# Performance work log

Hardware: AMD Instinct MI355X
Metric: run time of the kernel (lower is better)

The kernel has to match this reference:

```python
import jax, jax.numpy as jnp
import numpy as np

D_MODEL = 2048
NHEADS = 16
NOPE = 128
ROPE = 64
VDIM = 128
QLORA = 1536
KVLORA = 512
QHD = NOPE + ROPE  # 192
B, T = 1, 4096


def rms_norm(x, w):
    # torch.nn.RMSNorm with eps=None uses finfo(dtype).eps
    eps = jnp.finfo(x.dtype).eps
    var = jnp.mean(x * x, axis=-1, keepdims=True)
    return x * jax.lax.rsqrt(var + eps) * w


def rope_cos_sin(T, dim):
    freqs = 1.0 / (10000.0 ** (jnp.arange(0, dim, 2, dtype=jnp.float32) / dim))
    ang = jnp.arange(T, dtype=jnp.float32)[:, None] * freqs[None, :]  # (T, dim/2)
    return jnp.cos(ang), jnp.sin(ang)


def apply_rope(x, cos, sin):
    # interleaved RoPE: even/odd channel pairs rotated
    xe = x[..., 0::2]
    xo = x[..., 1::2]
    re = xe * cos - xo * sin
    ro = xo * cos + xe * sin
    return jnp.stack([re, ro], axis=-1).reshape(x.shape)


def setup_inputs() -> dict:
    key = jax.random.key(0)
    ks = jax.random.split(key, 6)
    s = 0.02
    return {
        "x": jax.random.normal(ks[0], (B, T, D_MODEL), jnp.float32),
        "Wqa": jax.random.normal(ks[1], (D_MODEL, QLORA), jnp.float32) * s,
        "q_ln_w": jnp.ones((QLORA,), jnp.float32),
        "Wqb": jax.random.normal(ks[2], (QLORA, NHEADS * QHD), jnp.float32) * s,
        "Wkva": jax.random.normal(ks[3], (D_MODEL, KVLORA + ROPE), jnp.float32) * s,
        "kv_ln_w": jnp.ones((KVLORA,), jnp.float32),
        "Wkvb": jax.random.normal(ks[4], (KVLORA, NHEADS * (NOPE + VDIM)), jnp.float32) * s,
        "Wo": jax.random.normal(ks[5], (NHEADS * VDIM, D_MODEL), jnp.float32) * s,
    }


def reference(x, Wqa, q_ln_w, Wqb, Wkva, kv_ln_w, Wkvb, Wo):
    Bx, Tx, _ = x.shape
    cos, sin = rope_cos_sin(Tx, ROPE)  # (T, ROPE/2)

    # Low-rank Q path
    q = rms_norm(x @ Wqa, q_ln_w) @ Wqb
    q = q.reshape(Bx, Tx, NHEADS, QHD).transpose(0, 2, 1, 3)  # (B,H,T,QHD)
    q_nope = q[..., :NOPE]
    q_rope = apply_rope(q[..., NOPE:], cos, sin)  # (B,H,T,ROPE)

    # Compressed KV path + shared rope key
    kv = x @ Wkva
    kv_c = kv[..., :KVLORA]  # (B,T,KVLORA) latent cache
    k_rope = apply_rope(kv[..., KVLORA:], cos, sin)  # (B,T,ROPE), head-shared

    kvb = (rms_norm(kv_c, kv_ln_w) @ Wkvb).reshape(Bx, Tx, NHEADS, NOPE + VDIM)
    k_nope = kvb[..., :NOPE].transpose(0, 2, 1, 3)  # (B,H,T,NOPE)
    v = kvb[..., NOPE:].transpose(0, 2, 1, 3)       # (B,H,T,VDIM)

    # Scores split into nope part + head-shared rope part (avoids expanding k_rope to H heads)
    scale = 1.0 / jnp.sqrt(jnp.float32(QHD))
    s = jnp.einsum('bhqd,bhkd->bhqk', q_nope, k_nope)
    s = s + jnp.einsum('bhqd,bkd->bhqk', q_rope, k_rope)
    s = s * scale

    mask = jnp.tril(jnp.ones((Tx, Tx), dtype=bool))
    s = jnp.where(mask, s, -jnp.inf)
    a = jax.nn.softmax(s, axis=-1)

    o = jnp.einsum('bhqk,bhkd->bhqd', a, v)
    o = o.transpose(0, 2, 1, 3).reshape(Bx, Tx, NHEADS * VDIM)
    return o @ Wo
```

## Files before the change

kernel.cpp:

```cpp
#include <hip/hip_runtime.h>
#include <hip/hip_bf16.h>

typedef __attribute__((ext_vector_type(8))) short short8;
typedef __attribute__((ext_vector_type(4))) float f32x4;

#define GLDS16(gp, lp)                                                         \
  __builtin_amdgcn_global_load_lds(                                            \
      (const __attribute__((address_space(1))) void*)(gp),                     \
      (__attribute__((address_space(3))) void*)(lp), 16, 0, 0)

static __device__ __forceinline__ unsigned int pack_bf16(float a, float b) {
  __hip_bfloat16 ba = __float2bfloat16(a), bb = __float2bfloat16(b);
  unsigned short ua = *reinterpret_cast<unsigned short*>(&ba);
  unsigned short ub = *reinterpret_cast<unsigned short*>(&bb);
  return (unsigned int)ua | ((unsigned int)ub << 16);
}

static __device__ __forceinline__ int xcd_swz(int linear, int nwg) {
  return (linear & 7) * (nwg >> 3) + (linear >> 3);
}

__global__ __launch_bounds__(256) void cast_bf16_kernel(
    const float* __restrict__ in, __hip_bfloat16* __restrict__ out, int n4)
{
  int i = blockIdx.x * 256 + threadIdx.x;
  if (i < n4) {
    float4 v = ((const float4*)in)[i];
    out[(size_t)i * 4 + 0] = __float2bfloat16(v.x);
    out[(size_t)i * 4 + 1] = __float2bfloat16(v.y);
    out[(size_t)i * 4 + 2] = __float2bfloat16(v.z);
    out[(size_t)i * 4 + 3] = __float2bfloat16(v.w);
  }
}

__global__ void transpose_cast_kernel(const float* __restrict__ in,
                                      __hip_bfloat16* __restrict__ out,
                                      int K, int N, int Npad)
{
  __shared__ float tile[32][33];
  int n0 = blockIdx.x * 32, k0 = blockIdx.y * 32;
  int tx = threadIdx.x, ty = threadIdx.y;
  #pragma unroll
  for (int i = ty; i < 32; i += 8) {
    int k = k0 + i, n = n0 + tx;
    tile[i][tx] = (n < N) ? in[(size_t)k * N + n] : 0.f;
  }
  __syncthreads();
  #pragma unroll
  for (int i = ty; i < 32; i += 8) {
    int n = n0 + i, k = k0 + tx;
    if (n < Npad) out[(size_t)n * K + k] = __float2bfloat16(tile[tx][i]);
  }
}

__global__ void rope_tab_kernel(float* __restrict__ cs, float* __restrict__ sn)
{
  int t = blockIdx.x, i = threadIdx.x;
  float freq = powf(10000.f, -2.f * (float)i / 64.f);
  float ang = (float)t * freq;
  cs[t * 32 + i] = cosf(ang);
  sn[t * 32 + i] = sinf(ang);
}

#define GEMM_MAIN(A, BT, Kdim)                                                 \
  __shared__ __hip_bfloat16 As[128 * 32];                                      \
  __shared__ __hip_bfloat16 Bs[128 * 32];                                      \
  const int tid = threadIdx.x;                                                 \
  const int wave = tid >> 6, lane = tid & 63;                                  \
  const int wr = wave >> 1, wc = wave & 1;                                     \
  const int lq = lane & 15, grp = lane >> 4;                                   \
  const int nwg = gridDim.x * gridDim.y;                                       \
  const int orig = xcd_swz(blockIdx.y * gridDim.x + blockIdx.x, nwg);          \
  const int row0 = (orig / gridDim.x) * 128;                                   \
  const int col0 = (orig % gridDim.x) * 128;                                   \
  const f32x4 z4 = {0.f, 0.f, 0.f, 0.f};                                       \
  f32x4 acc[4][4];                                                             \
  _Pragma("unroll") for (int i = 0; i < 4; i++)                                \
      _Pragma("unroll") for (int j = 0; j < 4; j++) acc[i][j] = z4;            \
  for (int k0 = 0; k0 < (Kdim); k0 += 32) {                                    \
    _Pragma("unroll") for (int i = 0; i < 2; i++) {                            \
      const int t = wave + 4 * i;                                              \
      const int c = t * 64 + lane;                                             \
      const int cr = c >> 2;                                                   \
      const int ko = (c & 3) << 3;                                             \
      GLDS16((A) + (size_t)(row0 + cr) * (Kdim) + (k0 + ko), (char*)As + t * 1024); \
      GLDS16((BT) + (size_t)(col0 + cr) * (Kdim) + (k0 + ko), (char*)Bs + t * 1024);\
    }                                                                          \
    __syncthreads();                                                           \
    short8 af[4], bfr[4];                                                      \
    _Pragma("unroll") for (int mm = 0; mm < 4; mm++)                           \
      af[mm] = *(const short8*)((const short*)As + ((wr * 64 + mm * 16 + lq) * 32 + grp * 8)); \
    _Pragma("unroll") for (int nn = 0; nn < 4; nn++)                           \
      bfr[nn] = *(const short8*)((const short*)Bs + ((wc * 64 + nn * 16 + lq) * 32 + grp * 8));\
    _Pragma("unroll") for (int mm = 0; mm < 4; mm++)                           \
      _Pragma("unroll") for (int nn = 0; nn < 4; nn++)                         \
        acc[mm][nn] = __builtin_amdgcn_mfma_f32_16x16x32_bf16(af[mm], bfr[nn], acc[mm][nn], 0, 0, 0); \
    __syncthreads();                                                           \
  }

__global__ __launch_bounds__(256) void gemm_bt_kernel(
    const __hip_bfloat16* __restrict__ A,
    const __hip_bfloat16* __restrict__ BT,
    float* __restrict__ C, int M, int N, int K)
{
  GEMM_MAIN(A, BT, K)
  #pragma unroll
  for (int mm = 0; mm < 4; mm++)
    #pragma unroll
    for (int nn = 0; nn < 4; nn++) {
      const int row = row0 + wr * 64 + mm * 16 + grp * 4;
      const int col = col0 + wc * 64 + nn * 16 + lq;
      float* Cp = C + (size_t)row * N + col;
      #pragma unroll
      for (int rr = 0; rr < 4; rr++) Cp[(size_t)rr * N] = acc[mm][nn][rr];
    }
}

#define GEMM256_MAIN(Aptr, BTptr, Kdim)                                        \
  __shared__ __align__(16) char Ab[2][32768];                                  \
  __shared__ __align__(16) char Bb[2][32768];                                  \
  const int tid = threadIdx.x;                                                 \
  const int wid = tid >> 6, lane = tid & 63;                                   \
  const int wm = wid >> 2, wn = wid & 3;                                       \
  const int lq = lane & 15, grp = lane >> 4;                                   \
  const int nwg = gridDim.x * gridDim.y;                                       \
  const int orig = xcd_swz(blockIdx.y * gridDim.x + blockIdx.x, nwg);          \
  const int row0 = (orig / gridDim.x) * 256;                                   \
  const int col0 = (orig % gridDim.x) * 256;                                   \
  const size_t K2 = (size_t)(Kdim) * 2;                                        \
  const char* pa[4]; const char* pb[4]; int ldst[4];                           \
  _Pragma("unroll") for (int i = 0; i < 4; i++) {                              \
    int L = i * 8192 + tid * 16;                                               \
    int r = L >> 7;                                                            \
    int csw = (L & 127) ^ ((r & 7) << 4);                                      \
    ldst[i] = L;                                                               \
    pa[i] = (const char*)(Aptr) + (size_t)(row0 + r) * K2 + csw;               \
    pb[i] = (const char*)(BTptr) + (size_t)(col0 + r) * K2 + csw;              \
  }                                                                            \
  const int xm = (lq & 7) << 4;                                                \
  const f32x4 z4 = {0.f, 0.f, 0.f, 0.f};                                       \
  f32x4 acc[8][4];                                                             \
  _Pragma("unroll") for (int i = 0; i < 8; i++)                                \
    _Pragma("unroll") for (int j = 0; j < 4; j++) acc[i][j] = z4;              \
  const int nt = (Kdim) >> 6;                                                  \
  _Pragma("unroll") for (int i = 0; i < 4; i++) {                              \
    GLDS16(pa[i], &Ab[0][0] + ldst[i]);                                        \
    GLDS16(pb[i], &Bb[0][0] + ldst[i]);                                        \
  }                                                                            \
  for (int t = 0; t < nt; ++t) {                                               \
    const int b = t & 1;                                                       \
    if (t + 1 < nt) {                                                          \
      const size_t koff = (size_t)(t + 1) * 128;                               \
      _Pragma("unroll") for (int i = 0; i < 4; i++) {                          \
        GLDS16(pa[i] + koff, &Ab[b ^ 1][0] + ldst[i]);                         \
        GLDS16(pb[i] + koff, &Bb[b ^ 1][0] + ldst[i]);                         \
      }                                                                        \
      asm volatile("s_waitcnt vmcnt(8)" ::: "memory");                         \
    } else {                                                                   \
      asm volatile("s_waitcnt vmcnt(0)" ::: "memory");                         \
    }                                                                          \
    __builtin_amdgcn_sched_barrier(0);                                         \
    __builtin_amdgcn_s_barrier();             \
    __builtin_amdgcn_sched_barrier(0);                                         \
    const char* Ar = &Ab[b][0];                                                \
    const char* Br = &Bb[b][0];                                                \
    short8 bfr[4][2];                                                          \
    _Pragma("unroll") for (int n = 0; n < 4; n++)                              \
      _Pragma("unroll") for (int ks = 0; ks < 2; ks++)                         \
        bfr[n][ks] = *(const short8*)(Br + (wn * 64 + n * 16 + lq) * 128 +     \
                                      ((ks * 64 + grp * 16) ^ xm));            \
    _Pragma("unroll") for (int mh = 0; mh < 4; mh++) {                         \
      short8 af[2][2];                                                         \
      _Pragma("unroll") for (int mi = 0; mi < 2; mi++)                         \
        _Pragma("unroll") for (int ks = 0; ks < 2; ks++)                       \
          af[mi][ks] = *(const short8*)(Ar + (wm * 128 + (mh * 2 + mi) * 16 + lq) * 128 + \
                                        ((ks * 64 + grp * 16) ^ xm));          \
      __builtin_amdgcn_s_setprio(1);                                           \
      _Pragma("unroll") for (int mi = 0; mi < 2; mi++)                         \
        _Pragma("unroll") for (int n = 0; n < 4; n++)                          \
          _Pragma("unroll") for (int ks = 0; ks < 2; ks++)                     \
            acc[mh * 2 + mi][n] = __builtin_amdgcn_mfma_f32_16x16x32_bf16(     \
                af[mi][ks], bfr[n][ks], acc[mh * 2 + mi][n], 0, 0, 0);         \
      __builtin_amdgcn_s_setprio(0);                                           \
    }                                                                          \
    __builtin_amdgcn_sched_barrier(0);                                         \
    __builtin_amdgcn_s_barrier();             \
    __builtin_amdgcn_sched_barrier(0);                                         \
  }

__global__ __launch_bounds__(512, 2) void gemm256_bt_kernel(
    const __hip_bfloat16* __restrict__ A,
    const __hip_bfloat16* __restrict__ BT,
    float* __restrict__ C, int N, int K)
{
  GEMM256_MAIN(A, BT, K)
  #pragma unroll
  for (int m = 0; m < 8; m++)
    #pragma unroll
    for (int n = 0; n < 4; n++) {
      const int row = row0 + wm * 128 + m * 16 + grp * 4;
      const int col = col0 + wn * 64 + n * 16 + lq;
      float* Cp = C + (size_t)row * N + col;
      #pragma unroll
      for (int rr = 0; rr < 4; rr++) Cp[(size_t)rr * N] = acc[m][n][rr];
    }
}

__global__ __launch_bounds__(512, 2) void gemm256_qup_kernel(
    const __hip_bfloat16* __restrict__ A,
    const __hip_bfloat16* __restrict__ BT,
    __hip_bfloat16* __restrict__ Qh,
    const float* __restrict__ cs_tab, const float* __restrict__ sn_tab, int K)
{
  GEMM256_MAIN(A, BT, K)
  const float scale = 0.10411654209f;
  #pragma unroll
  for (int m = 0; m < 8; m++)
    #pragma unroll
    for (int n = 0; n < 4; n++) {
      const int col = col0 + wn * 64 + n * 16 + lq;
      const int h = col / 192;
      const int d = col - h * 192;
      const bool is_rope = (d >= 128);
      const int i = (d - 128) >> 1;
      const float sgn = (d & 1) ? 1.f : -1.f;
      #pragma unroll
      for (int rr = 0; rr < 4; rr++) {
        const int t = row0 + wm * 128 + m * 16 + grp * 4 + rr;
        float val = acc[m][n][rr];
        float partner = __shfl_xor(val, 1);
        float outv = val;
        if (is_rope) {
          float c = cs_tab[t * 32 + i];
          float s = sn_tab[t * 32 + i];
          outv = val * c + sgn * partner * s;
        }
        Qh[((size_t)h * 4096 + t) * 192 + d] = __float2bfloat16(outv * scale);
      }
    }
}

__global__ __launch_bounds__(512, 2) void gemm256_kvup_kernel(
    const __hip_bfloat16* __restrict__ A,
    const __hip_bfloat16* __restrict__ BT,
    __hip_bfloat16* __restrict__ Kh,
    __hip_bfloat16* __restrict__ Vt, int K)
{
  GEMM256_MAIN(A, BT, K)
  #pragma unroll
  for (int m = 0; m < 8; m++)
    #pragma unroll
    for (int n = 0; n < 4; n++) {
      const int col = col0 + wn * 64 + n * 16 + lq;
      const int h = col >> 8;
      const int j = col & 255;
      const int t0 = row0 + wm * 128 + m * 16 + grp * 4;
      if (j < 128) {
        #pragma unroll
        for (int rr = 0; rr < 4; rr++)
          Kh[((size_t)h * 4096 + t0 + rr) * 192 + j] = __float2bfloat16(acc[m][n][rr]);
      } else {
        const int vd = j - 128;
        uint2 w;
        w.x = pack_bf16(acc[m][n][0], acc[m][n][1]);
        w.y = pack_bf16(acc[m][n][2], acc[m][n][3]);
        *(uint2*)(Vt + ((size_t)h * 128 + vd) * 4096 + t0) = w;
      }
    }
}

__global__ __launch_bounds__(256) void rmsnorm_cast_kernel(
    const float* __restrict__ in, int ld_in, const float* __restrict__ w,
    __hip_bfloat16* __restrict__ out, int W)
{
  const int row = blockIdx.x;
  const int tid = threadIdx.x;
  const int wave = tid >> 6, lane = tid & 63;
  const float* x = in + (size_t)row * ld_in;
  float ss = 0.f;
  for (int i = tid; i < W; i += 256) { float v = x[i]; ss += v * v; }
  #pragma unroll
  for (int o = 32; o; o >>= 1) ss += __shfl_xor(ss, o);
  __shared__ float red[4];
  __shared__ float stot;
  if (lane == 0) red[wave] = ss;
  __syncthreads();
  if (tid == 0) stot = red[0] + red[1] + red[2] + red[3];
  __syncthreads();
  const float rstd = rsqrtf(stot / (float)W + 1.1920929e-7f);
  for (int i = tid; i < W; i += 256)
    out[(size_t)row * W + i] = __float2bfloat16(x[i] * rstd * w[i]);
}

__global__ void rope_k_kernel(const float* __restrict__ kv, __hip_bfloat16* __restrict__ kr)
{
  int t = blockIdx.x;
  int i = threadIdx.x;
  if (i < 32) {
    float freq = powf(10000.f, -2.f * (float)i / 64.f);
    float ang = (float)t * freq;
    float c = cosf(ang), s = sinf(ang);
    float xe = kv[(size_t)t * 640 + 512 + 2 * i];
    float xo = kv[(size_t)t * 640 + 512 + 2 * i + 1];
    kr[(size_t)t * 64 + 2 * i]     = __float2bfloat16(xe * c - xo * s);
    kr[(size_t)t * 64 + 2 * i + 1] = __float2bfloat16(xo * c + xe * s);
  }
}

__global__ __launch_bounds__(256) void prep_krope_kernel(
    const __hip_bfloat16* __restrict__ kr, __hip_bfloat16* __restrict__ Kh)
{
  const int t = blockIdx.x;
  const int tid = threadIdx.x;
  for (int e = tid; e < 1024; e += 256) {
    int h = e >> 6, d = e & 63;
    Kh[((size_t)h * 4096 + t) * 192 + 128 + d] = kr[(size_t)t * 64 + d];
  }
}

__global__ __launch_bounds__(256, 2) void flash_attn_kernel(
    const __hip_bfloat16* __restrict__ Qh,
    const __hip_bfloat16* __restrict__ Kh,
    const __hip_bfloat16* __restrict__ Vt,
    __hip_bfloat16* __restrict__ Obf)
{
  __shared__ __align__(16) char Klds[2][24576];
  __shared__ __align__(16) char Vlds[2][16384];

  const int hw = blockIdx.x;
  const int rest = hw >> 3;
  const int h = (hw & 7) + 8 * (rest & 1);
  const int p = rest >> 1;

  const int wave = threadIdx.x >> 6;
  const int lane = threadIdx.x & 63;
  const int lq = lane & 15;
  const int grp = lane >> 4;
  const int qb_[2] = {(63 - p) * 64 + wave * 16,
                      p * 64 + wave * 16};
  const int kendA = qb_[0] + 16;
  const int kendB = qb_[1] + 16;
  const int nt = 64 - p;

  const char* Kh_ = (const char*)(Kh + (size_t)h * 4096 * 192);
  const char* Vh_ = (const char*)(Vt + (size_t)h * 128 * 4096);
  const short* Qh_ = (const short*)Qh + (size_t)h * 4096 * 192;

  int kbase[6], vbase[4];
  #pragma unroll
  for (int i = 0; i < 6; i++) {
    int L = (wave * 6 + i) * 1024 + lane * 16;
    int r = L / 384, c = L - r * 384;
    int swb = (r & 3) | (((r >> 3) & 1) << 2);
    kbase[i] = r * 384 + (c ^ (swb << 4));
  }
  #pragma unroll
  for (int i = 0; i < 4; i++) {
    int L = (wave * 4 + i) * 1024 + lane * 16;
    int r = L >> 7, c = L & 127;
    vbase[i] = r * 8192 + (c ^ ((r & 7) << 4));
  }

  short8 qf[2][6];
  #pragma unroll
  for (int f = 0; f < 2; f++)
    #pragma unroll
    for (int d = 0; d < 6; d++)
      qf[f][d] = *(const short8*)(Qh_ + (size_t)(qb_[f] + lq) * 192 + d * 32 + grp * 8);

  const f32x4 z4 = {0.f, 0.f, 0.f, 0.f};
  f32x4 o_acc[2][8];
  #pragma unroll
  for (int f = 0; f < 2; f++)
    #pragma unroll
    for (int v = 0; v < 8; v++) o_acc[f][v] = z4;
  float m[2] = {-1e30f, -1e30f};
  float lsum[2] = {0.f, 0.f};

  const int krow_l = ((lq >> 2) << 3) + (lq & 3);
  const int kxm = ((lq & 3) | (((lq >> 2) & 1) << 2)) << 4;
  const int vxm = (lq & 7) << 4;

  {
    #pragma unroll
    for (int i = 0; i < 6; i++) GLDS16(Kh_ + kbase[i], Klds[0] + (wave * 6 + i) * 1024);
    #pragma unroll
    for (int i = 0; i < 4; i++) GLDS16(Vh_ + vbase[i], Vlds[0] + (wave * 4 + i) * 1024);
  }

  for (int t = 0; t < nt; t++) {
    __syncthreads();
    if (t + 1 < nt) {
      const char* Kp = Kh_ + (size_t)(t + 1) * 64 * 384;
      const char* Vp = Vh_ + (size_t)(t + 1) * 128;
      char* Kd = Klds[(t + 1) & 1];
      char* Vd = Vlds[(t + 1) & 1];
      #pragma unroll
      for (int i = 0; i < 6; i++) GLDS16(Kp + kbase[i], Kd + (wave * 6 + i) * 1024);
      #pragma unroll
      for (int i = 0; i < 4; i++) GLDS16(Vp + vbase[i], Vd + (wave * 4 + i) * 1024);
    }
    const char* Kb = Klds[t & 1];
    const char* Vb = Vlds[t & 1];
    const int ks = t * 64;

    #pragma unroll
    for (int h2 = 0; h2 < 2; h2++) {
      const int ks32 = ks + h2 * 32;
      if (ks32 >= kendA) continue;
      const bool act1 = (ks32 < kendB);

      f32x4 st[2][2];
      #pragma unroll
      for (int kt = 0; kt < 2; kt++) {
        const int row = h2 * 32 + krow_l + kt * 4;
        short8 kf[6];
        #pragma unroll
        for (int d = 0; d < 6; d++)
          kf[d] = *(const short8*)(Kb + row * 384 + ((d * 64 + grp * 16) ^ kxm));
        #pragma unroll
        for (int f = 0; f < 2; f++) {
          if (f == 1 && !act1) continue;
          f32x4 acc = z4;
          #pragma unroll
          for (int d = 0; d < 6; d++)
            acc = __builtin_amdgcn_mfma_f32_16x16x32_bf16(kf[d], qf[f][d], acc, 0, 0, 0);
          st[f][kt] = acc;
        }
      }

      short8 vf[8];
      #pragma unroll
      for (int v = 0; v < 8; v++)
        vf[v] = *(const short8*)(Vb + (v * 16 + lq) * 128 + ((h2 * 64 + grp * 16) ^ vxm));

      #pragma unroll
      for (int f = 0; f < 2; f++) {
        if (f == 1 && !act1) continue;
        const int qg = qb_[f] + lq;
        const bool need_mask = (ks32 + 31 > qb_[f]);
        if (need_mask) {
          #pragma unroll
          for (int kt = 0; kt < 2; kt++)
            #pragma unroll
            for (int r = 0; r < 4; r++) {
              int key = ks32 + grp * 8 + kt * 4 + r;
              if (key > qg) st[f][kt][r] = -1e30f;
            }
        }
        float tmax = fmaxf(fmaxf(fmaxf(st[f][0][0], st[f][0][1]), fmaxf(st[f][0][2], st[f][0][3])),
                           fmaxf(fmaxf(st[f][1][0], st[f][1][1]), fmaxf(st[f][1][2], st[f][1][3])));
        tmax = fmaxf(tmax, __shfl_xor(tmax, 16));
        tmax = fmaxf(tmax, __shfl_xor(tmax, 32));
        if (!__all(tmax <= m[f] + 11.5416f)) {
          float mnew = fmaxf(m[f], tmax);
          float alpha = exp2f(m[f] - mnew);
          m[f] = mnew;
          lsum[f] *= alpha;
          float a0 = __shfl(alpha, grp * 4 + 0);
          float a1 = __shfl(alpha, grp * 4 + 1);
          float a2 = __shfl(alpha, grp * 4 + 2);
          float a3 = __shfl(alpha, grp * 4 + 3);
          #pragma unroll
          for (int v = 0; v < 8; v++) {
            o_acc[f][v][0] *= a0; o_acc[f][v][1] *= a1;
            o_acc[f][v][2] *= a2; o_acc[f][v][3] *= a3;
          }
        }
        float p00 = exp2f(st[f][0][0] - m[f]), p01 = exp2f(st[f][0][1] - m[f]);
        float p02 = exp2f(st[f][0][2] - m[f]), p03 = exp2f(st[f][0][3] - m[f]);
        float p10 = exp2f(st[f][1][0] - m[f]), p11 = exp2f(st[f][1][1] - m[f]);
        float p12 = exp2f(st[f][1][2] - m[f]), p13 = exp2f(st[f][1][3] - m[f]);
        float psum = ((p00 + p01) + (p02 + p03)) + ((p10 + p11) + (p12 + p13));
        psum += __shfl_xor(psum, 16);
        psum += __shfl_xor(psum, 32);
        lsum[f] += psum;
        union { unsigned int u[4]; short8 s8; } pu;
        pu.u[0] = pack_bf16(p00, p01);
        pu.u[1] = pack_bf16(p02, p03);
        pu.u[2] = pack_bf16(p10, p11);
        pu.u[3] = pack_bf16(p12, p13);
        short8 pa = pu.s8;
        #pragma unroll
        for (int v = 0; v < 8; v++)
          o_acc[f][v] = __builtin_amdgcn_mfma_f32_16x16x32_bf16(pa, vf[v], o_acc[f][v], 0, 0, 0);
      }
    }
  }

  #pragma unroll
  for (int f = 0; f < 2; f++) {
    float linv = 1.f / lsum[f];
    float l0 = __shfl(linv, grp * 4 + 0);
    float l1 = __shfl(linv, grp * 4 + 1);
    float l2 = __shfl(linv, grp * 4 + 2);
    float l3 = __shfl(linv, grp * 4 + 3);
    const int qb = qb_[f];
    #pragma unroll
    for (int v = 0; v < 8; v++) {
      int col = h * 128 + v * 16 + lq;
      Obf[(size_t)(qb + grp * 4 + 0) * 2048 + col] = __float2bfloat16(o_acc[f][v][0] * l0);
      Obf[(size_t)(qb + grp * 4 + 1) * 2048 + col] = __float2bfloat16(o_acc[f][v][1] * l1);
      Obf[(size_t)(qb + grp * 4 + 2) * 2048 + col] = __float2bfloat16(o_acc[f][v][2] * l2);
      Obf[(size_t)(qb + grp * 4 + 3) * 2048 + col] = __float2bfloat16(o_acc[f][v][3] * l3);
    }
  }
}

extern "C" void kernel_launch(void* const* d_in, const int* in_sizes, int n_in,
                              void* d_out, int out_size, void* d_ws, size_t ws_size,
                              hipStream_t stream)
{
  (void)in_sizes; (void)n_in; (void)out_size; (void)ws_size;
  const float* x     = (const float*)d_in[0];
  const float* Wqa   = (const float*)d_in[1];
  const float* qlnw  = (const float*)d_in[2];
  const float* Wqb   = (const float*)d_in[3];
  const float* Wkva  = (const float*)d_in[4];
  const float* kvlnw = (const float*)d_in[5];
  const float* Wkvb  = (const float*)d_in[6];
  const float* Wo    = (const float*)d_in[7];
  float* out = (float*)d_out;
  char* ws = (char*)d_ws;

  size_t off = 0;
  auto take = [&](size_t bytes) {
    char* p = ws + off;
    off += (bytes + 255) & ~(size_t)255;
    return p;
  };

  __hip_bfloat16* x_bf  = (__hip_bfloat16*)take((size_t)4096 * 2048 * 2);
  __hip_bfloat16* WqaT  = (__hip_bfloat16*)take((size_t)1536 * 2048 * 2);
  __hip_bfloat16* WqbT  = (__hip_bfloat16*)take((size_t)3072 * 1536 * 2);
  __hip_bfloat16* WkvaT = (__hip_bfloat16*)take((size_t)640 * 2048 * 2);
  __hip_bfloat16* WkvbT = (__hip_bfloat16*)take((size_t)4096 * 512 * 2);
  __hip_bfloat16* WoT   = (__hip_bfloat16*)take((size_t)2048 * 2048 * 2);
  char* regA            = take((size_t)4096 * 1536 * 4);
  float* kv             = (float*)take((size_t)4096 * 640 * 4);
  __hip_bfloat16* q_ln  = (__hip_bfloat16*)take((size_t)4096 * 1536 * 2);
  __hip_bfloat16* kv_ln = (__hip_bfloat16*)take((size_t)4096 * 512 * 2);
  __hip_bfloat16* kr    = (__hip_bfloat16*)take((size_t)4096 * 64 * 2);
  float* cs_tab         = (float*)take((size_t)4096 * 32 * 4);
  float* sn_tab         = (float*)take((size_t)4096 * 32 * 4);
  __hip_bfloat16* Khp   = (__hip_bfloat16*)take((size_t)16 * 4096 * 192 * 2);
  __hip_bfloat16* Vtp   = (__hip_bfloat16*)take((size_t)16 * 128 * 4096 * 2);
  __hip_bfloat16* o_bf  = (__hip_bfloat16*)take((size_t)4096 * 2048 * 2);

  float* q_lat = (float*)regA;
  __hip_bfloat16* Qh = (__hip_bfloat16*)regA;

  cast_bf16_kernel<<<dim3(8192), 256, 0, stream>>>(x, x_bf, 2097152);
  transpose_cast_kernel<<<dim3(48, 64), dim3(32, 8), 0, stream>>>(Wqa, WqaT, 2048, 1536, 1536);
  transpose_cast_kernel<<<dim3(96, 48), dim3(32, 8), 0, stream>>>(Wqb, WqbT, 1536, 3072, 3072);
  transpose_cast_kernel<<<dim3(20, 64), dim3(32, 8), 0, stream>>>(Wkva, WkvaT, 2048, 576, 640);
  transpose_cast_kernel<<<dim3(128, 16), dim3(32, 8), 0, stream>>>(Wkvb, WkvbT, 512, 4096, 4096);
  transpose_cast_kernel<<<dim3(64, 64), dim3(32, 8), 0, stream>>>(Wo, WoT, 2048, 2048, 2048);
  rope_tab_kernel<<<dim3(4096), 32, 0, stream>>>(cs_tab, sn_tab);

  gemm_bt_kernel<<<dim3(12, 32), 256, 0, stream>>>(x_bf, WqaT, q_lat, 4096, 1536, 2048);
  gemm_bt_kernel<<<dim3(5, 32), 256, 0, stream>>>(x_bf, WkvaT, kv, 4096, 640, 2048);

  rmsnorm_cast_kernel<<<dim3(4096), 256, 0, stream>>>(q_lat, 1536, qlnw, q_ln, 1536);
  rmsnorm_cast_kernel<<<dim3(4096), 256, 0, stream>>>(kv, 640, kvlnw, kv_ln, 512);
  rope_k_kernel<<<dim3(4096), 64, 0, stream>>>(kv, kr);

  gemm256_qup_kernel<<<dim3(12, 16), 512, 0, stream>>>(q_ln, WqbT, Qh, cs_tab, sn_tab, 1536);
  gemm256_kvup_kernel<<<dim3(16, 16), 512, 0, stream>>>(kv_ln, WkvbT, Khp, Vtp, 512);
  prep_krope_kernel<<<dim3(4096), 256, 0, stream>>>(kr, Khp);

  flash_attn_kernel<<<dim3(512), 256, 0, stream>>>(Qh, Khp, Vtp, o_bf);

  gemm256_bt_kernel<<<dim3(8, 16), 512, 0, stream>>>(o_bf, WoT, out, 2048, 2048);
}
```

Before: 479.9 us.

## Fuse down-projection GEMMs, merge norms and rope-K, load V fragments directly

Concatenates Wqa and Wkva into one transposed weight so a single GEMM produces both q_lat and kv. The two RMSNorm launches become one, and k-rope is written straight into the K buffer from precomputed tables, which removes the intermediate kr buffer and prep kernel. In the flash attention kernel, V is no longer staged through LDS; each lane reads its V fragments directly from global memory, and the K double-buffer is synchronised with explicit waitcnt and barriers. These changes cut launch count and LDS traffic, but direct global V loads may add latency in the attention inner loop.

```diff
diff --git a/kernel.cpp b/kernel.cpp
--- a/kernel.cpp
+++ b/kernel.cpp
@@ -98,21 +98,23 @@
     __syncthreads();                                                           \
   }
 
-__global__ __launch_bounds__(256) void gemm_bt_kernel(
+__global__ __launch_bounds__(256) void gemm_down_kernel(
     const __hip_bfloat16* __restrict__ A,
     const __hip_bfloat16* __restrict__ BT,
-    float* __restrict__ C, int M, int N, int K)
-{
-  GEMM_MAIN(A, BT, K)
+    float* __restrict__ q_lat, float* __restrict__ kvout)
+{
+  GEMM_MAIN(A, BT, 2048)
   #pragma unroll
   for (int mm = 0; mm < 4; mm++)
     #pragma unroll
     for (int nn = 0; nn < 4; nn++) {
       const int row = row0 + wr * 64 + mm * 16 + grp * 4;
       const int col = col0 + wc * 64 + nn * 16 + lq;
-      float* Cp = C + (size_t)row * N + col;
+      float* Cp = (col < 1536) ? (q_lat + (size_t)row * 1536 + col)
+                               : (kvout + (size_t)row * 640 + (col - 1536));
+      const size_t ld = (col < 1536) ? 1536 : 640;
       #pragma unroll
-      for (int rr = 0; rr < 4; rr++) Cp[(size_t)rr * N] = acc[mm][nn][rr];
+      for (int rr = 0; rr < 4; rr++) Cp[(size_t)rr * ld] = acc[mm][nn][rr];
     }
 }
 
@@ -269,14 +271,21 @@
     }
 }
 
-__global__ __launch_bounds__(256) void rmsnorm_cast_kernel(
-    const float* __restrict__ in, int ld_in, const float* __restrict__ w,
-    __hip_bfloat16* __restrict__ out, int W)
-{
-  const int row = blockIdx.x;
+__global__ __launch_bounds__(256) void rmsnorm2_kernel(
+    const float* __restrict__ q_lat, const float* __restrict__ kv,
+    const float* __restrict__ qw, const float* __restrict__ kvw,
+    __hip_bfloat16* __restrict__ q_ln, __hip_bfloat16* __restrict__ kv_ln)
+{
+  const int b = blockIdx.x;
+  const bool isq = (b < 4096);
+  const int row = isq ? b : b - 4096;
+  const int ld = isq ? 1536 : 640;
+  const int W = isq ? 1536 : 512;
+  const float* x = (isq ? q_lat : kv) + (size_t)row * ld;
+  const float* w = isq ? qw : kvw;
+  __hip_bfloat16* out = (isq ? q_ln : kv_ln) + (size_t)row * W;
   const int tid = threadIdx.x;
   const int wave = tid >> 6, lane = tid & 63;
-  const float* x = in + (size_t)row * ld_in;
   float ss = 0.f;
   for (int i = tid; i < W; i += 256) { float v = x[i]; ss += v * v; }
   #pragma unroll
@@ -289,32 +298,23 @@
   __syncthreads();
   const float rstd = rsqrtf(stot / (float)W + 1.1920929e-7f);
   for (int i = tid; i < W; i += 256)
-    out[(size_t)row * W + i] = __float2bfloat16(x[i] * rstd * w[i]);
-}
-
-__global__ void rope_k_kernel(const float* __restrict__ kv, __hip_bfloat16* __restrict__ kr)
-{
-  int t = blockIdx.x;
-  int i = threadIdx.x;
-  if (i < 32) {
-    float freq = powf(10000.f, -2.f * (float)i / 64.f);
-    float ang = (float)t * freq;
-    float c = cosf(ang), s = sinf(ang);
+    out[i] = __float2bfloat16(x[i] * rstd * w[i]);
+}
+
+__global__ __launch_bounds__(256) void ropek_direct_kernel(
+    const float* __restrict__ kv, const float* __restrict__ cs_tab,
+    const float* __restrict__ sn_tab, __hip_bfloat16* __restrict__ Kh)
+{
+  const int t = blockIdx.x;
+  const int tid = threadIdx.x;
+  for (int e = tid; e < 512; e += 256) {
+    int h = e >> 5, i = e & 31;
+    float c = cs_tab[t * 32 + i], s = sn_tab[t * 32 + i];
     float xe = kv[(size_t)t * 640 + 512 + 2 * i];
     float xo = kv[(size_t)t * 640 + 512 + 2 * i + 1];
-    kr[(size_t)t * 64 + 2 * i]     = __float2bfloat16(xe * c - xo * s);
-    kr[(size_t)t * 64 + 2 * i + 1] = __float2bfloat16(xo * c + xe * s);
-  }
-}
-
-__global__ __launch_bounds__(256) void prep_krope_kernel(
-    const __hip_bfloat16* __restrict__ kr, __hip_bfloat16* __restrict__ Kh)
-{
-  const int t = blockIdx.x;
-  const int tid = threadIdx.x;
-  for (int e = tid; e < 1024; e += 256) {
-    int h = e >> 6, d = e & 63;
-    Kh[((size_t)h * 4096 + t) * 192 + 128 + d] = kr[(size_t)t * 64 + d];
+    size_t base = ((size_t)h * 4096 + t) * 192 + 128 + 2 * i;
+    Kh[base]     = __float2bfloat16(xe * c - xo * s);
+    Kh[base + 1] = __float2bfloat16(xo * c + xe * s);
   }
 }
 
@@ -325,7 +325,6 @@
     __hip_bfloat16* __restrict__ Obf)
 {
   __shared__ __align__(16) char Klds[2][24576];
-  __shared__ __align__(16) char Vlds[2][16384];
 
   const int hw = blockIdx.x;
   const int rest = hw >> 3;
@@ -343,10 +342,10 @@
   const int nt = 64 - p;
 
   const char* Kh_ = (const char*)(Kh + (size_t)h * 4096 * 192);
-  const char* Vh_ = (const char*)(Vt + (size_t)h * 128 * 4096);
   const short* Qh_ = (const short*)Qh + (size_t)h * 4096 * 192;
-
-  int kbase[6], vbase[4];
+  const short* Vg = (const short*)Vt + (size_t)h * 128 * 4096 + (size_t)lq * 4096 + grp * 8;
+
+  int kbase[6];
   #pragma unroll
   for (int i = 0; i < 6; i++) {
     int L = (wave * 6 + i) * 1024 + lane * 16;
@@ -354,12 +353,6 @@
     int swb = (r & 3) | (((r >> 3) & 1) << 2);
     kbase[i] = r * 384 + (c ^ (swb << 4));
   }
-  #pragma unroll
-  for (int i = 0; i < 4; i++) {
-    int L = (wave * 4 + i) * 1024 + lane * 16;
-    int r = L >> 7, c = L & 127;
-    vbase[i] = r * 8192 + (c ^ ((r & 7) << 4));
-  }
 
   short8 qf[2][6];
   #pragma unroll
@@ -379,114 +372,111 @@
 
   const int krow_l = ((lq >> 2) << 3) + (lq & 3);
   const int kxm = ((lq & 3) | (((lq >> 2) & 1) << 2)) << 4;
-  const int vxm = (lq & 7) << 4;
-
-  {
-    #pragma unroll
-    for (int i = 0; i < 6; i++) GLDS16(Kh_ + kbase[i], Klds[0] + (wave * 6 + i) * 1024);
-    #pragma unroll
-    for (int i = 0; i < 4; i++) GLDS16(Vh_ + vbase[i], Vlds[0] + (wave * 4 + i) * 1024);
-  }
+
+#define ATTN_STEP(KS32, VF, H2)                                                \
+  if ((KS32) < kendA) {                                                        \
+    const bool act1 = ((KS32) < kendB);                                        \
+    f32x4 st[2][2];                                                            \
+    _Pragma("unroll") for (int kt = 0; kt < 2; kt++) {                         \
+      const int row = (H2) * 32 + krow_l + kt * 4;                             \
+      short8 kf[6];                                                            \
+      _Pragma("unroll") for (int d = 0; d < 6; d++)                            \
+        kf[d] = *(const short8*)(Kb + row * 384 + ((d * 64 + grp * 16) ^ kxm));\
+      _Pragma("unroll") for (int f = 0; f < 2; f++) {                          \
+        if (f == 1 && !act1) continue;                                         \
+        f32x4 a2 = z4;                                                         \
+        _Pragma("unroll") for (int d = 0; d < 6; d++)                          \
+          a2 = __builtin_amdgcn_mfma_f32_16x16x32_bf16(kf[d], qf[f][d], a2, 0, 0, 0); \
+        st[f][kt] = a2;                                                        \
+      }                                                                        \
+    }                                                                          \
+    _Pragma("unroll") for (int f = 0; f < 2; f++) {                            \
+      if (f == 1 && !act1) continue;                                           \
+      const int qg = qb_[f] + lq;                                              \
+      const bool need_mask = ((KS32) + 31 > qb_[f]);                           \
+      if (need_mask) {                                                         \
+        _Pragma("unroll") for (int kt = 0; kt < 2; kt++)                       \
+          _Pragma("unroll") for (int r = 0; r < 4; r++) {                      \
+            int key = (KS32) + grp * 8 + kt * 4 + r;                           \
+            if (key > qg) st[f][kt][r] = -1e30f;                               \
+          }                                                                    \
+      }                                                                        \
+      float tmax = fmaxf(fmaxf(fmaxf(st[f][0][0], st[f][0][1]), fmaxf(st[f][0][2], st[f][0][3])), \
+                         fmaxf(fmaxf(st[f][1][0], st[f][1][1]), fmaxf(st[f][1][2], st[f][1][3]))); \
+      tmax = fmaxf(tmax, __shfl_xor(tmax, 16));                                \
+      tmax = fmaxf(tmax, __shfl_xor(tmax, 32));                                \
+      if (!__all(tmax <= m[f] + 11.5416f)) {                                   \
+        float mnew = fmaxf(m[f], tmax);                                        \
+        float alpha = exp2f(m[f] - mnew);                                      \
+        m[f] = mnew;                                                           \
+        lsum[f] *= alpha;                                                      \
+        float a0 = __shfl(alpha, grp * 4 + 0);                                 \
+        float a1 = __shfl(alpha, grp * 4 + 1);                                 \
+        float a2s = __shfl(alpha, grp * 4 + 2);                                \
+        float a3 = __shfl(alpha, grp * 4 + 3);                                 \
+        _Pragma("unroll") for (int v = 0; v < 8; v++) {                        \
+          o_acc[f][v][0] *= a0; o_acc[f][v][1] *= a1;                          \
+          o_acc[f][v][2] *= a2s; o_acc[f][v][3] *= a3;                         \
+        }                                                                      \
+      }                                                                        \
+      float p00 = exp2f(st[f][0][0] - m[f]), p01 = exp2f(st[f][0][1] - m[f]);  \
+      float p02 = exp2f(st[f][0][2] - m[f]), p03 = exp2f(st[f][0][3] - m[f]);  \
+      float p10 = exp2f(st[f][1][0] - m[f]), p11 = exp2f(st[f][1][1] - m[f]);  \
+      float p12 = exp2f(st[f][1][2] - m[f]), p13 = exp2f(st[f][1][3] - m[f]);  \
+      float psum = ((p00 + p01) + (p02 + p03)) + ((p10 + p11) + (p12 + p13));  \
+      psum += __shfl_xor(psum, 16);                                            \
+      psum += __shfl_xor(psum, 32);                                            \
+      lsum[f] += psum;                                                         \
+      union { unsigned int u[4]; short8 s8; } pu;                              \
+      pu.u[0] = pack_bf16(p00, p01);                                           \
+      pu.u[1] = pack_bf16(p02, p03);                                           \
+      pu.u[2] = pack_bf16(p10, p11);                                           \
+      pu.u[3] = pack_bf16(p12, p13);                                           \
+      short8 pa = pu.s8;                                                       \
+      _Pragma("unroll") for (int v = 0; v < 8; v++)                            \
+        o_acc[f][v] = __builtin_amdgcn_mfma_f32_16x16x32_bf16(pa, (VF)[v], o_acc[f][v], 0, 0, 0); \
+    }                                                                          \
+  }
+
+  #pragma unroll
+  for (int i = 0; i < 6; i++) GLDS16(Kh_ + kbase[i], Klds[0] + (wave * 6 + i) * 1024);
+  asm volatile("s_waitcnt vmcnt(0)" ::: "memory");
+  __builtin_amdgcn_s_barrier();
 
   for (int t = 0; t < nt; t++) {
-    __syncthreads();
+    const char* Kb = Klds[t & 1];
+    const int ks = t * 64;
+
+    short8 vf0[8];
+    #pragma unroll
+    for (int v = 0; v < 8; v++)
+      vf0[v] = *(const short8*)(Vg + (size_t)v * 16 * 4096 + ks);
+    __builtin_amdgcn_sched_barrier(0);
+
+    ATTN_STEP(ks, vf0, 0)
+
+    short8 vf1[8];
+    #pragma unroll
+    for (int v = 0; v < 8; v++)
+      vf1[v] = *(const short8*)(Vg + (size_t)v * 16 * 4096 + ks + 32);
+    __builtin_amdgcn_sched_barrier(0);
+
     if (t + 1 < nt) {
-      const char* Kp = Kh_ + (size_t)(t + 1) * 64 * 384;
-      const char* Vp = Vh_ + (size_t)(t + 1) * 128;
+      const char* Kp = Kh_ + (size_t)(t + 1) * 24576;
       char* Kd = Klds[(t + 1) & 1];
-      char* Vd = Vlds[(t + 1) & 1];
       #pragma unroll
       for (int i = 0; i < 6; i++) GLDS16(Kp + kbase[i], Kd + (wave * 6 + i) * 1024);
-      #pragma unroll
-      for (int i = 0; i < 4; i++) GLDS16(Vp + vbase[i], Vd + (wave * 4 + i) * 1024);
     }
-    const char* Kb = Klds[t & 1];
-    const char* Vb = Vlds[t & 1];
-    const int ks = t * 64;
-
-    #pragma unroll
-    for (int h2 = 0; h2 < 2; h2++) {
-      const int ks32 = ks + h2 * 32;
-      if (ks32 >= kendA) continue;
-      const bool act1 = (ks32 < kendB);
-
-      f32x4 st[2][2];
-      #pragma unroll
-      for (int kt = 0; kt < 2; kt++) {
-        const int row = h2 * 32 + krow_l + kt * 4;
-        short8 kf[6];
-        #pragma unroll
-        for (int d = 0; d < 6; d++)
-          kf[d] = *(const short8*)(Kb + row * 384 + ((d * 64 + grp * 16) ^ kxm));
-        #pragma unroll
-        for (int f = 0; f < 2; f++) {
-          if (f == 1 && !act1) continue;
-          f32x4 acc = z4;
-          #pragma unroll
-          for (int d = 0; d < 6; d++)
-            acc = __builtin_amdgcn_mfma_f32_16x16x32_bf16(kf[d], qf[f][d], acc, 0, 0, 0);
-          st[f][kt] = acc;
-        }
-      }
-
-      short8 vf[8];
-      #pragma unroll
-      for (int v = 0; v < 8; v++)
-        vf[v] = *(const short8*)(Vb + (v * 16 + lq) * 128 + ((h2 * 64 + grp * 16) ^ vxm));
-
-      #pragma unroll
-      for (int f = 0; f < 2; f++) {
-        if (f == 1 && !act1) continue;
-        const int qg = qb_[f] + lq;
-        const bool need_mask = (ks32 + 31 > qb_[f]);
-        if (need_mask) {
-          #pragma unroll
-          for (int kt = 0; kt < 2; kt++)
-            #pragma unroll
-            for (int r = 0; r < 4; r++) {
-              int key = ks32 + grp * 8 + kt * 4 + r;
-              if (key > qg) st[f][kt][r] = -1e30f;
-            }
-        }
-        float tmax = fmaxf(fmaxf(fmaxf(st[f][0][0], st[f][0][1]), fmaxf(st[f][0][2], st[f][0][3])),
-                           fmaxf(fmaxf(st[f][1][0], st[f][1][1]), fmaxf(st[f][1][2], st[f][1][3])));
-        tmax = fmaxf(tmax, __shfl_xor(tmax, 16));
-        tmax = fmaxf(tmax, __shfl_xor(tmax, 32));
-        if (!__all(tmax <= m[f] + 11.5416f)) {
-          float mnew = fmaxf(m[f], tmax);
-          float alpha = exp2f(m[f] - mnew);
-          m[f] = mnew;
-          lsum[f] *= alpha;
-          float a0 = __shfl(alpha, grp * 4 + 0);
-          float a1 = __shfl(alpha, grp * 4 + 1);
-          float a2 = __shfl(alpha, grp * 4 + 2);
-          float a3 = __shfl(alpha, grp * 4 + 3);
-          #pragma unroll
-          for (int v = 0; v < 8; v++) {
-            o_acc[f][v][0] *= a0; o_acc[f][v][1] *= a1;
-            o_acc[f][v][2] *= a2; o_acc[f][v][3] *= a3;
-          }
-        }
-        float p00 = exp2f(st[f][0][0] - m[f]), p01 = exp2f(st[f][0][1] - m[f]);
-        float p02 = exp2f(st[f][0][2] - m[f]), p03 = exp2f(st[f][0][3] - m[f]);
-        float p10 = exp2f(st[f][1][0] - m[f]), p11 = exp2f(st[f][1][1] - m[f]);
-        float p12 = exp2f(st[f][1][2] - m[f]), p13 = exp2f(st[f][1][3] - m[f]);
-        float psum = ((p00 + p01) + (p02 + p03)) + ((p10 + p11) + (p12 + p13));
-        psum += __shfl_xor(psum, 16);
-        psum += __shfl_xor(psum, 32);
-        lsum[f] += psum;
-        union { unsigned int u[4]; short8 s8; } pu;
-        pu.u[0] = pack_bf16(p00, p01);
-        pu.u[1] = pack_bf16(p02, p03);
-        pu.u[2] = pack_bf16(p10, p11);
-        pu.u[3] = pack_bf16(p12, p13);
-        short8 pa = pu.s8;
-        #pragma unroll
-        for (int v = 0; v < 8; v++)
-          o_acc[f][v] = __builtin_amdgcn_mfma_f32_16x16x32_bf16(pa, vf[v], o_acc[f][v], 0, 0, 0);
-      }
-    }
-  }
+    __builtin_amdgcn_sched_barrier(0);
+
+    ATTN_STEP(ks + 32, vf1, 1)
+
+    __builtin_amdgcn_sched_barrier(0);
+    asm volatile("s_waitcnt vmcnt(0)" ::: "memory");
+    __builtin_amdgcn_sched_barrier(0);
+    __builtin_amdgcn_s_barrier();
+  }
+#undef ATTN_STEP
 
   #pragma unroll
   for (int f = 0; f < 2; f++) {
@@ -530,44 +520,39 @@
     return p;
   };
 
-  __hip_bfloat16* x_bf  = (__hip_bfloat16*)take((size_t)4096 * 2048 * 2);
-  __hip_bfloat16* WqaT  = (__hip_bfloat16*)take((size_t)1536 * 2048 * 2);
-  __hip_bfloat16* WqbT  = (__hip_bfloat16*)take((size_t)3072 * 1536 * 2);
-  __hip_bfloat16* WkvaT = (__hip_bfloat16*)take((size_t)640 * 2048 * 2);
-  __hip_bfloat16* WkvbT = (__hip_bfloat16*)take((size_t)4096 * 512 * 2);
-  __hip_bfloat16* WoT   = (__hip_bfloat16*)take((size_t)2048 * 2048 * 2);
-  char* regA            = take((size_t)4096 * 1536 * 4);
-  float* kv             = (float*)take((size_t)4096 * 640 * 4);
-  __hip_bfloat16* q_ln  = (__hip_bfloat16*)take((size_t)4096 * 1536 * 2);
-  __hip_bfloat16* kv_ln = (__hip_bfloat16*)take((size_t)4096 * 512 * 2);
-  __hip_bfloat16* kr    = (__hip_bfloat16*)take((size_t)4096 * 64 * 2);
-  float* cs_tab         = (float*)take((size_t)4096 * 32 * 4);
-  float* sn_tab         = (float*)take((size_t)4096 * 32 * 4);
-  __hip_bfloat16* Khp   = (__hip_bfloat16*)take((size_t)16 * 4096 * 192 * 2);
-  __hip_bfloat16* Vtp   = (__hip_bfloat16*)take((size_t)16 * 128 * 4096 * 2);
-  __hip_bfloat16* o_bf  = (__hip_bfloat16*)take((size_t)4096 * 2048 * 2);
+  __hip_bfloat16* x_bf   = (__hip_bfloat16*)take((size_t)4096 * 2048 * 2);
+  __hip_bfloat16* WdownT = (__hip_bfloat16*)take((size_t)2176 * 2048 * 2);
+  __hip_bfloat16* WqbT   = (__hip_bfloat16*)take((size_t)3072 * 1536 * 2);
+  __hip_bfloat16* WkvbT  = (__hip_bfloat16*)take((size_t)4096 * 512 * 2);
+  __hip_bfloat16* WoT    = (__hip_bfloat16*)take((size_t)2048 * 2048 * 2);
+  char* regA             = take((size_t)4096 * 1536 * 4);
+  float* kv              = (float*)take((size_t)4096 * 640 * 4);
+  __hip_bfloat16* q_ln   = (__hip_bfloat16*)take((size_t)4096 * 1536 * 2);
+  __hip_bfloat16* kv_ln  = (__hip_bfloat16*)take((size_t)4096 * 512 * 2);
+  float* cs_tab          = (float*)take((size_t)4096 * 32 * 4);
+  float* sn_tab          = (float*)take((size_t)4096 * 32 * 4);
+  __hip_bfloat16* Khp    = (__hip_bfloat16*)take((size_t)16 * 4096 * 192 * 2);
+  __hip_bfloat16* Vtp    = (__hip_bfloat16*)take((size_t)16 * 128 * 4096 * 2);
+  __hip_bfloat16* o_bf   = (__hip_bfloat16*)take((size_t)4096 * 2048 * 2);
 
   float* q_lat = (float*)regA;
   __hip_bfloat16* Qh = (__hip_bfloat16*)regA;
 
   cast_bf16_kernel<<<dim3(8192), 256, 0, stream>>>(x, x_bf, 2097152);
-  transpose_cast_kernel<<<dim3(48, 64), dim3(32, 8), 0, stream>>>(Wqa, WqaT, 2048, 1536, 1536);
+  transpose_cast_kernel<<<dim3(48, 64), dim3(32, 8), 0, stream>>>(Wqa, WdownT, 2048, 1536, 1536);
+  transpose_cast_kernel<<<dim3(20, 64), dim3(32, 8), 0, stream>>>(Wkva, WdownT + (size_t)1536 * 2048, 2048, 576, 640);
   transpose_cast_kernel<<<dim3(96, 48), dim3(32, 8), 0, stream>>>(Wqb, WqbT, 1536, 3072, 3072);
-  transpose_cast_kernel<<<dim3(20, 64), dim3(32, 8), 0, stream>>>(Wkva, WkvaT, 2048, 576, 640);
   transpose_cast_kernel<<<dim3(128, 16), dim3(32, 8), 0, stream>>>(Wkvb, WkvbT, 512, 4096, 4096);
   transpose_cast_kernel<<<dim3(64, 64), dim3(32, 8), 0, stream>>>(Wo, WoT, 2048, 2048, 2048);
   rope_tab_kernel<<<dim3(4096), 32, 0, stream>>>(cs_tab, sn_tab);
 
-  gemm_bt_kernel<<<dim3(12, 32), 256, 0, stream>>>(x_bf, WqaT, q_lat, 4096, 1536, 2048);
-  gemm_bt_kernel<<<dim3(5, 32), 256, 0, stream>>>(x_bf, WkvaT, kv, 4096, 640, 2048);
-
-  rmsnorm_cast_kernel<<<dim3(4096), 256, 0, stream>>>(q_lat, 1536, qlnw, q_ln, 1536);
-  rmsnorm_cast_kernel<<<dim3(4096), 256, 0, stream>>>(kv, 640, kvlnw, kv_ln, 512);
-  rope_k_kernel<<<dim3(4096), 64, 0, stream>>>(kv, kr);
+  gemm_down_kernel<<<dim3(17, 32), 256, 0, stream>>>(x_bf, WdownT, q_lat, kv);
+
+  rmsnorm2_kernel<<<dim3(8192), 256, 0, stream>>>(q_lat, kv, qlnw, kvlnw, q_ln, kv_ln);
+  ropek_direct_kernel<<<dim3(4096), 256, 0, stream>>>(kv, cs_tab, sn_tab, Khp);
 
   gemm256_qup_kernel<<<dim3(12, 16), 512, 0, stream>>>(q_ln, WqbT, Qh, cs_tab, sn_tab, 1536);
   gemm256_kvup_kernel<<<dim3(16, 16), 512, 0, stream>>>(kv_ln, WkvbT, Khp, Vtp, 512);
-  prep_krope_kernel<<<dim3(4096), 256, 0, stream>>>(kr, Khp);
 
   flash_attn_kernel<<<dim3(512), 256, 0, stream>>>(Qh, Khp, Vtp, o_bf);
 
```

After: 562.6 us. +17.2%, slower.
